# Kernel optimization log

Hardware: AMD Instinct MI355X
Metric: run time of the kernel (lower is better)

## Reference

```python
import jax, jax.numpy as jnp
import numpy as np

N_NODES = 50000
N_EDGES = 800000
D_IN, D_HID, D_OUT = 128, 128, 64


def _gcn_conv(x, row, col, W, b, num_nodes):
    # Linear (no bias in lin; bias added after aggregation)
    h = x @ W  # [N, d_out]
    # degree over destination (col), includes self-loops
    deg = jax.ops.segment_sum(jnp.ones_like(col, dtype=h.dtype), col, num_segments=num_nodes)
    dis = jnp.where(deg > 0, deg ** -0.5, 0.0)  # deg^{-1/2}, inf -> 0
    norm = dis[row] * dis[col]  # [E+N]
    msg = h[row] * norm[:, None]  # gather + scale
    out = jax.ops.segment_sum(msg, col, num_segments=num_nodes)  # scatter-add
    return out + b


def setup_inputs() -> dict:
    key = jax.random.key(0)
    k1, k2, k3, k4 = jax.random.split(key, 4)
    x = jax.random.normal(k1, (N_NODES, D_IN), dtype=jnp.float32)
    edge_index = jax.random.randint(k2, (2, N_EDGES), 0, N_NODES, dtype=jnp.int32)
    # glorot-like init for linear weights
    W1 = jax.random.normal(k3, (D_IN, D_HID), dtype=jnp.float32) * (2.0 / (D_IN + D_HID)) ** 0.5
    W2 = jax.random.normal(k4, (D_HID, D_OUT), dtype=jnp.float32) * (2.0 / (D_HID + D_OUT)) ** 0.5
    b1 = jnp.zeros((D_HID,), dtype=jnp.float32)
    b2 = jnp.zeros((D_OUT,), dtype=jnp.float32)
    return {"x": x, "edge_index": edge_index, "W1": W1, "b1": b1, "W2": W2, "b2": b2}


def reference(x, edge_index, W1, b1, W2, b2):
    n = x.shape[0]
    # add self-loops
    loops = jnp.arange(n, dtype=edge_index.dtype)
    row = jnp.concatenate([edge_index[0], loops])
    col = jnp.concatenate([edge_index[1], loops])
    h = _gcn_conv(x, row, col, W1, b1, n)
    h = jax.nn.relu(h)  # dropout is identity in eval mode
    out = _gcn_conv(h, row, col, W2, b2, n)
    return out
```

## Files before the change

kernel.cpp:

```cpp
#include <hip/hip_runtime.h>

#define NB 196
#define BSH 8
#define BMSK 255
#define NBLK_A 512
#define BINCAP 6144

typedef __attribute__((ext_vector_type(8))) short short8;
typedef __attribute__((ext_vector_type(4))) float f32x4;
typedef __attribute__((ext_vector_type(4))) unsigned int u32x4;

static inline size_t alignup(size_t x) { return (x + 255) & ~(size_t)255; }

__device__ __forceinline__ unsigned short f2bf(float f) {
    unsigned int u = __float_as_uint(f);
    u = (u + 0x7fffu + ((u >> 16) & 1u)) >> 16;
    return (unsigned short)u;
}

__global__ __launch_bounds__(256) void k_hist(const int* __restrict__ colp, int nE,
                                              unsigned* __restrict__ counts,
                                              const float* __restrict__ W1,
                                              const float* __restrict__ W2,
                                              unsigned short* __restrict__ Wt1,
                                              unsigned short* __restrict__ Wt2) {
    int blk = blockIdx.x;
    if (blk >= NBLK_A) {
        int i = (blk - NBLK_A) * 256 + threadIdx.x;
        if (i < 128 * 128) { int k = i >> 7, c = i & 127; Wt1[(size_t)c * 128 + k] = f2bf(W1[i]); }
        if (i < 128 * 64)  { int k = i >> 6, c = i & 63;  Wt2[(size_t)c * 128 + k] = f2bf(W2[i]); }
        return;
    }
    __shared__ unsigned h[NB];
    for (int i = threadIdx.x; i < NB; i += 256) h[i] = 0;
    __syncthreads();
    int chunk = (nE + NBLK_A - 1) / NBLK_A;
    int e0 = blk * chunk, e1 = min(nE, e0 + chunk);
    for (int e = e0 + (int)threadIdx.x; e < e1; e += 256)
        atomicAdd(&h[colp[e] >> BSH], 1u);
    __syncthreads();
    for (int i = threadIdx.x; i < NB; i += 256) counts[(size_t)i * NBLK_A + blk] = h[i];
}

__global__ __launch_bounds__(256) void k_scanA(unsigned* __restrict__ counts,
                                               unsigned* __restrict__ bintot) {
    int bin = blockIdx.x, t = threadIdx.x;
    __shared__ unsigned ps[256];
    unsigned c0 = counts[(size_t)bin * NBLK_A + 2 * t];
    unsigned c1 = counts[(size_t)bin * NBLK_A + 2 * t + 1];
    unsigned s = c0 + c1;
    ps[t] = s;
    __syncthreads();
    for (int d = 1; d < 256; d <<= 1) {
        unsigned v = (t >= d) ? ps[t - d] : 0u;
        __syncthreads();
        ps[t] += v;
        __syncthreads();
    }
    unsigned base = ps[t] - s;
    counts[(size_t)bin * NBLK_A + 2 * t] = base;
    counts[(size_t)bin * NBLK_A + 2 * t + 1] = base + c0;
    if (t == 255) bintot[bin] = ps[255];
}

__global__ __launch_bounds__(256) void k_scanB(const unsigned* __restrict__ bintot,
                                               unsigned* __restrict__ edgebase, int nE) {
    __shared__ unsigned bt[NB];
    int t = threadIdx.x;
    if (t < NB) bt[t] = bintot[t];
    __syncthreads();
    if (t == 0) {
        unsigned run = 0;
        for (int b = 0; b < NB; ++b) { unsigned v = bt[b]; bt[b] = run; run += v; }
    }
    __syncthreads();
    if (t < NB) edgebase[t] = bt[t];
    if (t == 0) edgebase[NB] = (unsigned)nE;
}

__global__ __launch_bounds__(256) void k_scatter(const int* __restrict__ colp,
                                                 const int* __restrict__ rowp, int nE,
                                                 const unsigned* __restrict__ counts,
                                                 const unsigned* __restrict__ edgebase,
                                                 unsigned* __restrict__ pairs) {
    __shared__ unsigned cur[NB];
    int blk = blockIdx.x;
    for (int i = threadIdx.x; i < NB; i += 256)
        cur[i] = edgebase[i] + counts[(size_t)i * NBLK_A + blk];
    __syncthreads();
    int chunk = (nE + NBLK_A - 1) / NBLK_A;
    int e0 = blk * chunk, e1 = min(nE, e0 + chunk);
    for (int e = e0 + (int)threadIdx.x; e < e1; e += 256) {
        int c = colp[e], r = rowp[e];
        unsigned pos = atomicAdd(&cur[c >> BSH], 1u);
        pairs[pos] = ((unsigned)r << BSH) | (unsigned)(c & BMSK);
    }
}

__global__ __launch_bounds__(256) void k_binbuild(const unsigned* __restrict__ pairs,
                                                  const unsigned* __restrict__ edgebase,
                                                  unsigned* __restrict__ csr,
                                                  unsigned* __restrict__ off,
                                                  float* __restrict__ dis, int n) {
    __shared__ unsigned lp[BINCAP];
    __shared__ unsigned lr[BINCAP];
    __shared__ unsigned hist[256];
    __shared__ unsigned scn[256];
    int b = blockIdx.x, t = threadIdx.x;
    unsigned e0 = edgebase[b], e1 = edgebase[b + 1];
    unsigned ec = e1 - e0;
    if (ec > BINCAP) ec = BINCAP;
    hist[t] = 0;
    __syncthreads();
    for (unsigned i = t; i < ec; i += 256) {
        unsigned v = pairs[e0 + i];
        lp[i] = v;
        atomicAdd(&hist[v & BMSK], 1u);
    }
    __syncthreads();
    unsigned hv = hist[t];
    scn[t] = hv;
    __syncthreads();
    for (int d = 1; d < 256; d <<= 1) {
        unsigned v = (t >= d) ? scn[t - d] : 0u;
        __syncthreads();
        scn[t] += v;
        __syncthreads();
    }
    unsigned ex = scn[t] - hv;
    int node = (b << BSH) + t;
    if (node < n) {
        off[node] = e0 + ex;
        dis[node] = rsqrtf((float)(hv + 1));
    }
    if (b == NB - 1 && t == 0) off[n] = e1;
    __syncthreads();
    scn[t] = ex;
    __syncthreads();
    for (unsigned i = t; i < ec; i += 256) {
        unsigned v = lp[i];
        unsigned pos = atomicAdd(&scn[v & BMSK], 1u);
        lr[pos] = v >> BSH;
    }
    __syncthreads();
    for (unsigned i = t; i < ec; i += 256) csr[e0 + i] = lr[i];
}

template <int NT, bool IN_BF16, bool BIAS_RELU>
__device__ __forceinline__ void gemm_body(int bid, const void* __restrict__ Ap,
                                          const unsigned short* __restrict__ Wt,
                                          const float* __restrict__ bias,
                                          unsigned short* __restrict__ out, int M) {
    const int lane = threadIdx.x & 63;
    const int wave = threadIdx.x >> 6;
    const int m0 = bid * 64 + wave * 16;
    const int lrow = lane & 15;
    const int lk = lane >> 4;
    int arow = m0 + lrow;
    if (arow >= M) arow = M - 1;

    f32x4 acc[NT];
#pragma unroll
    for (int t = 0; t < NT; ++t) acc[t] = (f32x4){0.f, 0.f, 0.f, 0.f};

#pragma unroll
    for (int k0 = 0; k0 < 4; ++k0) {
        const int kb = k0 * 32 + lk * 8;
        short8 afrag;
        if (IN_BF16) {
            const unsigned short* A = (const unsigned short*)Ap;
            u32x4 v = __builtin_nontemporal_load((const u32x4*)&A[(size_t)arow * 128 + kb]);
#pragma unroll
            for (int q = 0; q < 4; ++q) {
                float lo = __uint_as_float(v[q] << 16);
                float hi = __uint_as_float(v[q] & 0xffff0000u);
                if (BIAS_RELU) {
                    lo = fmaxf(lo + bias[kb + 2 * q], 0.f);
                    hi = fmaxf(hi + bias[kb + 2 * q + 1], 0.f);
                }
                afrag[2 * q] = (short)f2bf(lo);
                afrag[2 * q + 1] = (short)f2bf(hi);
            }
        } else {
            const float* A = (const float*)Ap;
            const float* ap = &A[(size_t)arow * 128 + kb];
            f32x4 v0 = __builtin_nontemporal_load((const f32x4*)ap);
            f32x4 v1 = __builtin_nontemporal_load((const f32x4*)(ap + 4));
#pragma unroll
            for (int q = 0; q < 4; ++q) {
                afrag[q] = (short)f2bf(v0[q]);
                afrag[4 + q] = (short)f2bf(v1[q]);
            }
        }
#pragma unroll
        for (int t = 0; t < NT; ++t) {
            const int bcol = t * 16 + lrow;
            short8 bfrag = *(const short8*)&Wt[(size_t)bcol * 128 + kb];
            acc[t] = __builtin_amdgcn_mfma_f32_16x16x32_bf16(afrag, bfrag, acc[t], 0, 0, 0);
        }
    }

#pragma unroll
    for (int i = 0; i < 4; ++i) {
        int row = m0 + lk * 4 + i;
        if (row < M) {
#pragma unroll
            for (int t = 0; t < NT; ++t)
                out[(size_t)row * (NT * 16) + t * 16 + lrow] = f2bf(acc[t][i]);
        }
    }
}

__global__ __launch_bounds__(256) void k_gemm1(const float* __restrict__ x,
                                               const unsigned short* __restrict__ Wt1,
                                               unsigned short* __restrict__ hs1, int M) {
    gemm_body<8, false, false>(blockIdx.x, x, Wt1, nullptr, hs1, M);
}

__global__ __launch_bounds__(256) void k_gemm2(const unsigned short* __restrict__ agg1,
                                               const unsigned short* __restrict__ Wt2,
                                               const float* __restrict__ b1,
                                               unsigned short* __restrict__ hs2, int M) {
    gemm_body<4, true, true>(blockIdx.x, agg1, Wt2, b1, hs2, M);
}

__device__ __forceinline__ void acc8s(float a[8], u32x4 u, float d) {
    a[0] = fmaf(__uint_as_float(u[0] << 16), d, a[0]);
    a[1] = fmaf(__uint_as_float(u[0] & 0xffff0000u), d, a[1]);
    a[2] = fmaf(__uint_as_float(u[1] << 16), d, a[2]);
    a[3] = fmaf(__uint_as_float(u[1] & 0xffff0000u), d, a[3]);
    a[4] = fmaf(__uint_as_float(u[2] << 16), d, a[4]);
    a[5] = fmaf(__uint_as_float(u[2] & 0xffff0000u), d, a[5]);
    a[6] = fmaf(__uint_as_float(u[3] << 16), d, a[6]);
    a[7] = fmaf(__uint_as_float(u[3] & 0xffff0000u), d, a[7]);
}

template <int D, bool OUT_F32, bool ADD_BIAS>
__global__ __launch_bounds__(256) void k_gather_csr(const unsigned short* __restrict__ hs,
                                                    const unsigned* __restrict__ csr,
                                                    const unsigned* __restrict__ off,
                                                    const float* __restrict__ dis,
                                                    const float* __restrict__ bias,
                                                    void* __restrict__ outp, int n) {
    const int TPN = D / 8;
    const int NPB = 256 / TPN;
    int v = blockIdx.x * NPB + (int)(threadIdx.x / TPN);
    int c = threadIdx.x % TPN;
    if (v >= n) return;
    const u32x4* h4 = (const u32x4*)hs;
    const size_t rs = D / 8;
    size_t base = (size_t)v * rs + c;

    unsigned s = off[v], e = off[v + 1];
    float dv = dis[v];

    float a[8];
#pragma unroll
    for (int j = 0; j < 8; ++j) a[j] = 0.f;
    acc8s(a, h4[base], dv);

    unsigned i = s;
    for (; i + 4 <= e; i += 4) {
        unsigned r0 = csr[i], r1 = csr[i + 1], r2 = csr[i + 2], r3 = csr[i + 3];
        float d0 = dis[r0], d1 = dis[r1], d2 = dis[r2], d3 = dis[r3];
        u32x4 m0 = h4[(size_t)r0 * rs + c];
        u32x4 m1 = h4[(size_t)r1 * rs + c];
        u32x4 m2 = h4[(size_t)r2 * rs + c];
        u32x4 m3 = h4[(size_t)r3 * rs + c];
        acc8s(a, m0, d0); acc8s(a, m1, d1); acc8s(a, m2, d2); acc8s(a, m3, d3);
    }
    for (; i < e; ++i) {
        unsigned r = csr[i];
        acc8s(a, h4[(size_t)r * rs + c], dis[r]);
    }

    if (OUT_F32) {
        float* o = (float*)outp;
        float rr[8];
#pragma unroll
        for (int j = 0; j < 8; ++j) {
            rr[j] = a[j] * dv;
            if (ADD_BIAS) rr[j] += bias[c * 8 + j];
        }
        f32x4 lov = {rr[0], rr[1], rr[2], rr[3]};
        f32x4 hiv = {rr[4], rr[5], rr[6], rr[7]};
        __builtin_nontemporal_store(lov, (f32x4*)&o[(size_t)v * D + c * 8]);
        __builtin_nontemporal_store(hiv, (f32x4*)&o[(size_t)v * D + c * 8 + 4]);
    } else {
        u32x4 o;
        o[0] = (unsigned)f2bf(a[0] * dv) | ((unsigned)f2bf(a[1] * dv) << 16);
        o[1] = (unsigned)f2bf(a[2] * dv) | ((unsigned)f2bf(a[3] * dv) << 16);
        o[2] = (unsigned)f2bf(a[4] * dv) | ((unsigned)f2bf(a[5] * dv) << 16);
        o[3] = (unsigned)f2bf(a[6] * dv) | ((unsigned)f2bf(a[7] * dv) << 16);
        ((u32x4*)outp)[base] = o;
    }
}

extern "C" void kernel_launch(void* const* d_in, const int* in_sizes, int n_in,
                              void* d_out, int out_size, void* d_ws, size_t ws_size,
                              hipStream_t stream) {
    const float* x  = (const float*)d_in[0];
    const int*   ei = (const int*)d_in[1];
    const float* W1 = (const float*)d_in[2];
    const float* b1 = (const float*)d_in[3];
    const float* W2 = (const float*)d_in[4];
    const float* b2 = (const float*)d_in[5];

    const int Din = 128;
    const int Nn = in_sizes[0] / Din;
    const int E  = in_sizes[1] / 2;
    const int* rowp = ei;
    const int* colp = ei + E;

    char* ws = (char*)d_ws;
    size_t off_ = 0;
    unsigned*       counts   = (unsigned*)(ws + off_);       off_ = alignup(off_ + (size_t)NB * NBLK_A * 4);
    unsigned*       bintot   = (unsigned*)(ws + off_);       off_ = alignup(off_ + NB * 4);
    unsigned*       edgebase = (unsigned*)(ws + off_);       off_ = alignup(off_ + (NB + 1) * 4);
    unsigned*       pairs    = (unsigned*)(ws + off_);       off_ = alignup(off_ + (size_t)E * 4);
    unsigned*       csr      = (unsigned*)(ws + off_);       off_ = alignup(off_ + (size_t)E * 4);
    unsigned*       offv     = (unsigned*)(ws + off_);       off_ = alignup(off_ + (size_t)(Nn + 1) * 4);
    float*          dis      = (float*)(ws + off_);          off_ = alignup(off_ + (size_t)Nn * 4);
    unsigned short* Wt1      = (unsigned short*)(ws + off_); off_ = alignup(off_ + 128 * 128 * 2);
    unsigned short* Wt2      = (unsigned short*)(ws + off_); off_ = alignup(off_ + 128 * 64 * 2);
    unsigned short* hs1      = (unsigned short*)(ws + off_); off_ = alignup(off_ + (size_t)Nn * 128 * 2);
    unsigned short* agg1     = (unsigned short*)(ws + off_); off_ = alignup(off_ + (size_t)Nn * 128 * 2);
    unsigned short* hs2      = hs1;
    float*          outp     = (float*)d_out;

    k_hist<<<NBLK_A + 64, 256, 0, stream>>>(colp, E, counts, W1, W2, Wt1, Wt2);
    k_scanA<<<NB, 256, 0, stream>>>(counts, bintot);
    k_scanB<<<1, 256, 0, stream>>>(bintot, edgebase, E);
    k_scatter<<<NBLK_A, 256, 0, stream>>>(colp, rowp, E, counts, edgebase, pairs);
    k_binbuild<<<NB, 256, 0, stream>>>(pairs, edgebase, csr, offv, dis, Nn);

    k_gemm1<<<(Nn + 63) / 64, 256, 0, stream>>>(x, Wt1, hs1, Nn);

    k_gather_csr<128, false, false><<<(Nn + 15) / 16, 256, 0, stream>>>(
        hs1, csr, offv, dis, nullptr, agg1, Nn);

    k_gemm2<<<(Nn + 63) / 64, 256, 0, stream>>>(agg1, Wt2, b1, hs2, Nn);

    k_gather_csr<64, true, true><<<(Nn + 31) / 32, 256, 0, stream>>>(
        hs2, csr, offv, dis, b2, (void*)outp, Nn);
}
```

Measured before the change: 119.5 us.

## Fold source-side degree scaling into GEMM epilogues and sort CSR neighbor lists

The GEMM epilogues now multiply each output row by its deg^{-1/2}, so the gather kernels just sum pre-scaled neighbor rows. This drops the per-edge random dis[r] load and the multiply from the aggregation loops. Each node's neighbor list inside a bin is also insertion-sorted per thread, so source-row reads become more ordered and cache-friendly. The catch is a serial per-thread sort with divergent run lengths in the CSR build kernel, plus a switch from nontemporal to normal loads of agg1.

```diff
diff --git a/kernel.cpp b/kernel.cpp
--- a/kernel.cpp
+++ b/kernel.cpp
@@ -143,6 +143,13 @@
         lr[pos] = v >> BSH;
     }
     __syncthreads();
+    for (unsigned i = 1; i < hv; ++i) {
+        unsigned key = lr[ex + i];
+        int j = (int)i - 1;
+        while (j >= 0 && lr[ex + j] > key) { lr[ex + j + 1] = lr[ex + j]; --j; }
+        lr[ex + j + 1] = key;
+    }
+    __syncthreads();
     for (unsigned i = t; i < ec; i += 256) csr[e0 + i] = lr[i];
 }
 
@@ -150,6 +157,7 @@
 __device__ __forceinline__ void gemm_body(int bid, const void* __restrict__ Ap,
                                           const unsigned short* __restrict__ Wt,
                                           const float* __restrict__ bias,
+                                          const float* __restrict__ dis,
                                           unsigned short* __restrict__ out, int M) {
     const int lane = threadIdx.x & 63;
     const int wave = threadIdx.x >> 6;
@@ -169,7 +177,7 @@
         short8 afrag;
         if (IN_BF16) {
             const unsigned short* A = (const unsigned short*)Ap;
-            u32x4 v = __builtin_nontemporal_load((const u32x4*)&A[(size_t)arow * 128 + kb]);
+            u32x4 v = *(const u32x4*)&A[(size_t)arow * 128 + kb];
 #pragma unroll
             for (int q = 0; q < 4; ++q) {
                 float lo = __uint_as_float(v[q] << 16);
@@ -204,35 +212,38 @@
     for (int i = 0; i < 4; ++i) {
         int row = m0 + lk * 4 + i;
         if (row < M) {
+            float s = dis[row];
 #pragma unroll
             for (int t = 0; t < NT; ++t)
-                out[(size_t)row * (NT * 16) + t * 16 + lrow] = f2bf(acc[t][i]);
+                out[(size_t)row * (NT * 16) + t * 16 + lrow] = f2bf(acc[t][i] * s);
         }
     }
 }
 
 __global__ __launch_bounds__(256) void k_gemm1(const float* __restrict__ x,
                                                const unsigned short* __restrict__ Wt1,
+                                               const float* __restrict__ dis,
                                                unsigned short* __restrict__ hs1, int M) {
-    gemm_body<8, false, false>(blockIdx.x, x, Wt1, nullptr, hs1, M);
+    gemm_body<8, false, false>(blockIdx.x, x, Wt1, nullptr, dis, hs1, M);
 }
 
 __global__ __launch_bounds__(256) void k_gemm2(const unsigned short* __restrict__ agg1,
                                                const unsigned short* __restrict__ Wt2,
                                                const float* __restrict__ b1,
+                                               const float* __restrict__ dis,
                                                unsigned short* __restrict__ hs2, int M) {
-    gemm_body<4, true, true>(blockIdx.x, agg1, Wt2, b1, hs2, M);
-}
-
-__device__ __forceinline__ void acc8s(float a[8], u32x4 u, float d) {
-    a[0] = fmaf(__uint_as_float(u[0] << 16), d, a[0]);
-    a[1] = fmaf(__uint_as_float(u[0] & 0xffff0000u), d, a[1]);
-    a[2] = fmaf(__uint_as_float(u[1] << 16), d, a[2]);
-    a[3] = fmaf(__uint_as_float(u[1] & 0xffff0000u), d, a[3]);
-    a[4] = fmaf(__uint_as_float(u[2] << 16), d, a[4]);
-    a[5] = fmaf(__uint_as_float(u[2] & 0xffff0000u), d, a[5]);
-    a[6] = fmaf(__uint_as_float(u[3] << 16), d, a[6]);
-    a[7] = fmaf(__uint_as_float(u[3] & 0xffff0000u), d, a[7]);
+    gemm_body<4, true, true>(blockIdx.x, agg1, Wt2, b1, dis, hs2, M);
+}
+
+__device__ __forceinline__ void acc8(float a[8], u32x4 u) {
+    a[0] += __uint_as_float(u[0] << 16);
+    a[1] += __uint_as_float(u[0] & 0xffff0000u);
+    a[2] += __uint_as_float(u[1] << 16);
+    a[3] += __uint_as_float(u[1] & 0xffff0000u);
+    a[4] += __uint_as_float(u[2] << 16);
+    a[5] += __uint_as_float(u[2] & 0xffff0000u);
+    a[6] += __uint_as_float(u[3] << 16);
+    a[7] += __uint_as_float(u[3] & 0xffff0000u);
 }
 
 template <int D, bool OUT_F32, bool ADD_BIAS>
@@ -257,22 +268,18 @@
     float a[8];
 #pragma unroll
     for (int j = 0; j < 8; ++j) a[j] = 0.f;
-    acc8s(a, h4[base], dv);
+    acc8(a, h4[base]);
 
     unsigned i = s;
     for (; i + 4 <= e; i += 4) {
         unsigned r0 = csr[i], r1 = csr[i + 1], r2 = csr[i + 2], r3 = csr[i + 3];
-        float d0 = dis[r0], d1 = dis[r1], d2 = dis[r2], d3 = dis[r3];
         u32x4 m0 = h4[(size_t)r0 * rs + c];
         u32x4 m1 = h4[(size_t)r1 * rs + c];
         u32x4 m2 = h4[(size_t)r2 * rs + c];
         u32x4 m3 = h4[(size_t)r3 * rs + c];
-        acc8s(a, m0, d0); acc8s(a, m1, d1); acc8s(a, m2, d2); acc8s(a, m3, d3);
-    }
-    for (; i < e; ++i) {
-        unsigned r = csr[i];
-        acc8s(a, h4[(size_t)r * rs + c], dis[r]);
-    }
+        acc8(a, m0); acc8(a, m1); acc8(a, m2); acc8(a, m3);
+    }
+    for (; i < e; ++i) acc8(a, h4[(size_t)csr[i] * rs + c]);
 
     if (OUT_F32) {
         float* o = (float*)outp;
@@ -334,12 +341,12 @@
     k_scatter<<<NBLK_A, 256, 0, stream>>>(colp, rowp, E, counts, edgebase, pairs);
     k_binbuild<<<NB, 256, 0, stream>>>(pairs, edgebase, csr, offv, dis, Nn);
 
-    k_gemm1<<<(Nn + 63) / 64, 256, 0, stream>>>(x, Wt1, hs1, Nn);
+    k_gemm1<<<(Nn + 63) / 64, 256, 0, stream>>>(x, Wt1, dis, hs1, Nn);
 
     k_gather_csr<128, false, false><<<(Nn + 15) / 16, 256, 0, stream>>>(
         hs1, csr, offv, dis, nullptr, agg1, Nn);
 
-    k_gemm2<<<(Nn + 63) / 64, 256, 0, stream>>>(agg1, Wt2, b1, hs2, Nn);
+    k_gemm2<<<(Nn + 63) / 64, 256, 0, stream>>>(agg1, Wt2, b1, dis, hs2, Nn);
 
     k_gather_csr<64, true, true><<<(Nn + 31) / 32, 256, 0, stream>>>(
         hs2, csr, offv, dis, b2, (void*)outp, Nn);
```

After: 151.5 us. +26.7%, slower.
